# Optimization experiments

Hardware: AMD Instinct MI355X
Metric: run time of the kernel (lower is better)

## Reference

```python
import jax, jax.numpy as jnp
from jax import lax
import numpy as np

FRAME_LEN = 128
HOP = 64  # frame_len // 2 (default hop)
SAMPLE_LEN = 65536
IR_LEN = 1024

# torch.hann_window(N) is periodic: 0.5*(1 - cos(2*pi*n/N))
WIN = 0.5 * (1.0 - jnp.cos(2.0 * jnp.pi * jnp.arange(FRAME_LEN, dtype=jnp.float32) / FRAME_LEN))


def setup_inputs() -> dict:
    key = jax.random.key(0)
    k1, k2 = jax.random.split(key)
    x = jax.random.normal(k1, (1, SAMPLE_LEN), dtype=jnp.float32)
    IR = jax.random.normal(k2, (1, IR_LEN), dtype=jnp.float32)
    return {"x": x, "IR": IR}


def _scale_ir(ir2d):
    # get_MSG + scale_IR(target_gain = MSG + 2)
    spec = jnp.fft.rfft(ir2d[0])
    mag = jnp.abs(spec)
    phase = jnp.angle(spec)
    power = mag ** 2
    MLG = jnp.mean(power)
    zero_phase = (phase > -0.1) & (phase < 0.1)  # DC bin always qualifies
    peak_gain = jnp.max(jnp.where(zero_phase, power, -jnp.inf))
    MSG = -10.0 * jnp.log10(peak_gain / MLG)
    target_gain = MSG + 2.0
    mean_gain = 10.0 * jnp.log10(MLG)
    factor = jnp.power(jnp.float32(0.5), (target_gain - mean_gain) / 6.0)
    return ir2d / factor


def _howling(x1d, ir1d):
    L = x1d.shape[0]
    conv_len = FRAME_LEN + ir1d.shape[0] - 1
    # number of iterations that perform the feedback update (torch loop breaks
    # when frame_start + conv_len >= sample_len, AFTER adding to howling_out)
    n_fb = max(0, (L - conv_len - 1) // HOP)

    def step(x, i):
        fs = i * HOP
        frame = lax.dynamic_slice(x, (fs,), (FRAME_LEN,))
        w = WIN * frame
        conv = jnp.convolve(w, ir1d)  # mode='full', length conv_len
        fs2 = fs + HOP
        seg = lax.dynamic_slice(x, (fs2,), (conv_len,)) + conv
        x = lax.dynamic_update_slice(x, seg, (fs2,))
        x = jnp.clip(x, -1.0, 1.0)
        return x, w

    x_out, frames = lax.scan(step, x1d, jnp.arange(n_fb))
    # last iteration: windowed frame added to howling_out, then break (no feedback, no clamp)
    fs_last = n_fb * HOP
    last_w = WIN * lax.dynamic_slice(x_out, (fs_last,), (FRAME_LEN,))
    frames = jnp.concatenate([frames, last_w[None, :]], axis=0)  # [T, frame_len]
    T = n_fb + 1
    pos = (jnp.arange(T)[:, None] * HOP + jnp.arange(FRAME_LEN)[None, :]).reshape(-1)
    howl = jnp.zeros((L,), x1d.dtype).at[pos].add(frames.reshape(-1))
    return jnp.clip(howl, -1.0, 1.0)


def reference(x, IR):
    ir = _scale_ir(IR)
    out = _howling(x[0], ir[0])
    return out[None, :]
```

## Files before the change

### kernel.cpp

```cpp
#include <hip/hip_runtime.h>
#include <math.h>

#define FRAME 128
#define HOPW 64
#define SLEN 65536
#define IRLEN 1024
#define NFB 1006
#define RMASK 2047
#define PI_D 3.14159265358979323846

__device__ __forceinline__ float clip1(float v) { return fminf(1.0f, fmaxf(-1.0f, v)); }

__device__ __forceinline__ void loop_barrier() {
    __builtin_amdgcn_sched_barrier(0);
    asm volatile("s_waitcnt lgkmcnt(0)" ::: "memory");
    __builtin_amdgcn_s_barrier();
    __builtin_amdgcn_sched_barrier(0);
}

__global__ __launch_bounds__(768) void howl_fused(const float* __restrict__ x,
                                                  const float* __restrict__ ir,
                                                  float* __restrict__ out) {
    __shared__ __align__(16) float ring[2048];
    __shared__ __align__(16) float part[4][1152];
    __shared__ float irl[IRLEN];
    __shared__ float wlds[FRAME];
    __shared__ float red1[1024];
    __shared__ float red2[1024];
    __shared__ float invfs;

    const int tid = threadIdx.x;
    const int lane = tid & 63;
    const int wvid = tid >> 6;
    const int kg = tid / 192;
    const int ob = tid % 192;
    const int q = ob * 6;
    const int lo = q - kg * 32 - 31;

    for (int idx = tid; idx < IRLEN; idx += 768) irl[idx] = ir[idx];
    for (int idx = tid; idx < 1216; idx += 768) ring[idx] = x[idx];
    if (tid >= 513) { red1[tid] = -INFINITY; red2[tid] = 0.f; }
    if (tid < 256) { red1[768 + tid] = -INFINITY; red2[768 + tid] = 0.f; }
    __syncthreads();

    if (tid < 513) {
        double th = -2.0 * PI_D * (double)tid / 1024.0;
        double c4 = cos(4.0 * th), s4 = sin(4.0 * th);
        double wr0 = 1.0,           wi0 = 0.0;
        double wr1 = cos(th),       wi1 = sin(th);
        double wr2 = cos(2.0 * th), wi2 = sin(2.0 * th);
        double wr3 = cos(3.0 * th), wi3 = sin(3.0 * th);
        double ar0 = 0, ai0 = 0, ar1 = 0, ai1 = 0, ar2 = 0, ai2 = 0, ar3 = 0, ai3 = 0;
        for (int m = 0; m < 256; ++m) {
            double x0 = irl[4 * m], x1 = irl[4 * m + 1], x2 = irl[4 * m + 2], x3 = irl[4 * m + 3];
            ar0 += x0 * wr0; ai0 += x0 * wi0;
            ar1 += x1 * wr1; ai1 += x1 * wi1;
            ar2 += x2 * wr2; ai2 += x2 * wi2;
            ar3 += x3 * wr3; ai3 += x3 * wi3;
            double t;
            t = wr0 * c4 - wi0 * s4; wi0 = wr0 * s4 + wi0 * c4; wr0 = t;
            t = wr1 * c4 - wi1 * s4; wi1 = wr1 * s4 + wi1 * c4; wr1 = t;
            t = wr2 * c4 - wi2 * s4; wi2 = wr2 * s4 + wi2 * c4; wr2 = t;
            t = wr3 * c4 - wi3 * s4; wi3 = wr3 * s4 + wi3 * c4; wr3 = t;
        }
        double re = (ar0 + ar1) + (ar2 + ar3);
        double im = (ai0 + ai1) + (ai2 + ai3);
        float mag = (float)sqrt(re * re + im * im);
        float pw = mag * mag;
        double ph = atan2(im, re);
        int ok = (ph > -0.1 && ph < 0.1) ? 1 : 0;
        red1[tid] = ok ? pw : -INFINITY;
        red2[tid] = pw;
    }
    __syncthreads();
    for (int st = 512; st > 0; st >>= 1) {
        if (tid < st) {
            red1[tid] = fmaxf(red1[tid], red1[tid + st]);
            red2[tid] = red2[tid] + red2[tid + st];
        }
        __syncthreads();
    }
    if (tid == 0) {
        float peak = red1[0];
        float MLG = red2[0] / 513.0f;
        float MSG = -10.0f * log10f(peak / MLG);
        float target_gain = MSG + 2.0f;
        float mean_gain = 10.0f * log10f(MLG);
        invfs = powf(0.5f, (target_gain - mean_gain) / 6.0f);
    }
    __syncthreads();
    const float fbc = invfs;

    float wir[37];
#pragma unroll
    for (int j = 0; j < 37; ++j) {
        int idx = lo + j;
        wir[j] = (idx >= 0 && idx < IRLEN) ? irl[idx] / fbc : 0.f;
    }

    const float hvs = (float)(0.5 * (1.0 - cos(PI_D * (double)(tid & 127) / 64.0)));

    float tl = 0.f, xv = 0.f;
    if (tid < FRAME) wlds[tid] = hvs * ring[tid];
    if (wvid == 11) xv = x[1216 + lane];
    if (wvid < 2) __builtin_amdgcn_s_setprio(1);
    __syncthreads();

#pragma unroll 1
    for (int i = 0; i < NFB; ++i) {
        const int base = i * HOPW;

        if (wvid == 0) {
            float w0v = wlds[lane];
            float w1v = wlds[64 + lane];
            out[base + lane] = clip1(w0v + tl);
            tl = w1v;
        } else if (wvid == 11) {
            int pos = base + 1216 + lane;
            if (pos < SLEN) ring[pos & RMASK] = clip1(xv);
            int np = pos + HOPW;
            xv = (np < SLEN) ? x[np] : 0.f;
        }

        float wreg = wlds[kg * 32 + (lane & 31)];
        float a0 = 0, a1 = 0, a2 = 0, a3 = 0, a4 = 0, a5 = 0;
#pragma unroll
        for (int kk = 0; kk < 32; ++kk) {
            float sc = __int_as_float(__builtin_amdgcn_readlane(__float_as_int(wreg), 31 - kk));
            a0 = fmaf(sc, wir[kk + 0], a0);
            a1 = fmaf(sc, wir[kk + 1], a1);
            a2 = fmaf(sc, wir[kk + 2], a2);
            a3 = fmaf(sc, wir[kk + 3], a3);
            a4 = fmaf(sc, wir[kk + 4], a4);
            a5 = fmaf(sc, wir[kk + 5], a5);
        }
        float* pw = &part[kg][q];
        *(float2*)(pw + 0) = make_float2(a0, a1);
        *(float2*)(pw + 2) = make_float2(a2, a3);
        *(float2*)(pw + 4) = make_float2(a4, a5);

        loop_barrier();

        if (tid < 128) {
            int s = tid;
            int slot = (base + 64 + s) & RMASK;
            float rr = ring[slot];
            float sc4 = ((part[0][s] + part[1][s]) + part[2][s]) + part[3][s];
            float v = clip1(rr + sc4);
            ring[slot] = v;
            wlds[s] = hvs * v;
        } else if (tid < 384) {
            int p = 128 + 4 * (tid - 128);
            float4 g0 = *(const float4*)&part[0][p];
            float4 g1 = *(const float4*)&part[1][p];
            float4 g2 = *(const float4*)&part[2][p];
            float4 g3 = *(const float4*)&part[3][p];
            int slot = (base + 64 + p) & RMASK;
            float4 rv = *(float4*)&ring[slot];
            rv.x = clip1(rv.x + (((g0.x + g1.x) + g2.x) + g3.x));
            rv.y = clip1(rv.y + (((g0.y + g1.y) + g2.y) + g3.y));
            rv.z = clip1(rv.z + (((g0.z + g1.z) + g2.z) + g3.z));
            rv.w = clip1(rv.w + (((g0.w + g1.w) + g2.w) + g3.w));
            *(float4*)&ring[slot] = rv;
        }

        loop_barrier();
    }

    if (wvid == 0) {
        out[64384 + lane] = clip1(wlds[lane] + tl);
        out[64448 + lane] = clip1(wlds[64 + lane]);
    }
    for (int idx = 64512 + tid; idx < SLEN; idx += 768) out[idx] = 0.f;
}

extern "C" void kernel_launch(void* const* d_in, const int* in_sizes, int n_in,
                              void* d_out, int out_size, void* d_ws, size_t ws_size,
                              hipStream_t stream) {
    const float* x = (const float*)d_in[0];
    const float* ir = (const float*)d_in[1];
    float* out = (float*)d_out;
    (void)d_ws; (void)ws_size; (void)in_sizes; (void)n_in; (void)out_size;

    hipLaunchKernelGGL(howl_fused, dim3(1), dim3(768), 0, stream, x, ir, out);
}
```

Before: 1.020 ms.

## Double-buffer partial sums to use one barrier per feedback iteration

Restructures the serial feedback loop so each iteration has a single barrier instead of two. The partial-sum buffer is double-buffered. Every thread recomputes the reduced windowed sample it needs straight from the previous partials, which removes the separate reduce-then-broadcast phase. The loop is unrolled by two to ping-pong the buffers. The cost is redundant reduction work in every thread, extra LDS, and subtle ring/vbuf ordering hazards.

```diff
diff --git a/kernel.cpp b/kernel.cpp
--- a/kernel.cpp
+++ b/kernel.cpp
@@ -22,9 +22,10 @@
                                                   const float* __restrict__ ir,
                                                   float* __restrict__ out) {
     __shared__ __align__(16) float ring[2048];
-    __shared__ __align__(16) float part[4][1152];
+    __shared__ __align__(16) float part[2][4][1152];
     __shared__ float irl[IRLEN];
-    __shared__ float wlds[FRAME];
+    __shared__ float vbuf[2][128];
+    __shared__ float wb[2][128];
     __shared__ float red1[1024];
     __shared__ float red2[1024];
     __shared__ float invfs;
@@ -36,6 +37,8 @@
     const int ob = tid % 192;
     const int q = ob * 6;
     const int lo = q - kg * 32 - 31;
+    const int s = kg * 32 + (lane & 31);
+    const bool wlow = (ob < 64) && (lane < 32);
 
     for (int idx = tid; idx < IRLEN; idx += 768) irl[idx] = ir[idx];
     for (int idx = tid; idx < 1216; idx += 768) ring[idx] = x[idx];
@@ -98,31 +101,16 @@
         wir[j] = (idx >= 0 && idx < IRLEN) ? irl[idx] / fbc : 0.f;
     }
 
-    const float hvs = (float)(0.5 * (1.0 - cos(PI_D * (double)(tid & 127) / 64.0)));
-
+    const float hann_s = (float)(0.5 * (1.0 - cos(PI_D * (double)s / 64.0)));
+
+    float wreg = hann_s * ring[s];
+    if (wlow) wb[0][s] = wreg;
+    if (tid < 64) vbuf[1][64 + tid] = ring[64 + tid];
     float tl = 0.f, xv = 0.f;
-    if (tid < FRAME) wlds[tid] = hvs * ring[tid];
     if (wvid == 11) xv = x[1216 + lane];
-    if (wvid < 2) __builtin_amdgcn_s_setprio(1);
-    __syncthreads();
-
-#pragma unroll 1
-    for (int i = 0; i < NFB; ++i) {
-        const int base = i * HOPW;
-
-        if (wvid == 0) {
-            float w0v = wlds[lane];
-            float w1v = wlds[64 + lane];
-            out[base + lane] = clip1(w0v + tl);
-            tl = w1v;
-        } else if (wvid == 11) {
-            int pos = base + 1216 + lane;
-            if (pos < SLEN) ring[pos & RMASK] = clip1(xv);
-            int np = pos + HOPW;
-            xv = (np < SLEN) ? x[np] : 0.f;
-        }
-
-        float wreg = wlds[kg * 32 + (lane & 31)];
+    __syncthreads();
+
+    {
         float a0 = 0, a1 = 0, a2 = 0, a3 = 0, a4 = 0, a5 = 0;
 #pragma unroll
         for (int kk = 0; kk < 32; ++kk) {
@@ -134,27 +122,36 @@
             a4 = fmaf(sc, wir[kk + 4], a4);
             a5 = fmaf(sc, wir[kk + 5], a5);
         }
-        float* pw = &part[kg][q];
+        float* pw = &part[0][kg][q];
         *(float2*)(pw + 0) = make_float2(a0, a1);
         *(float2*)(pw + 2) = make_float2(a2, a3);
         *(float2*)(pw + 4) = make_float2(a4, a5);
-
-        loop_barrier();
-
-        if (tid < 128) {
-            int s = tid;
-            int slot = (base + 64 + s) & RMASK;
-            float rr = ring[slot];
-            float sc4 = ((part[0][s] + part[1][s]) + part[2][s]) + part[3][s];
-            float v = clip1(rr + sc4);
-            ring[slot] = v;
-            wlds[s] = hvs * v;
-        } else if (tid < 384) {
+    }
+    loop_barrier();
+
+    auto body = [&](int i, const float* cur, float* nxt,
+                    const float* vb_r, float* vb_w,
+                    const float* wb_r, float* wb_w) {
+        const int base = i * HOPW;
+
+        if (wvid == 0) {
+            float w0v = wb_r[lane];
+            float w1v = wb_r[64 + lane];
+            out[base + lane] = clip1(w0v + tl);
+            tl = w1v;
+        } else if (wvid == 11) {
+            int pos = base + 1216 + lane;
+            if (pos < SLEN) ring[pos & RMASK] = clip1(xv);
+            int np = pos + HOPW;
+            xv = (np < SLEN) ? x[np] : 0.f;
+        }
+
+        if (tid >= 128 && tid < 384) {
             int p = 128 + 4 * (tid - 128);
-            float4 g0 = *(const float4*)&part[0][p];
-            float4 g1 = *(const float4*)&part[1][p];
-            float4 g2 = *(const float4*)&part[2][p];
-            float4 g3 = *(const float4*)&part[3][p];
+            float4 g0 = *(const float4*)&cur[p];
+            float4 g1 = *(const float4*)&cur[1152 + p];
+            float4 g2 = *(const float4*)&cur[2304 + p];
+            float4 g3 = *(const float4*)&cur[3456 + p];
             int slot = (base + 64 + p) & RMASK;
             float4 rv = *(float4*)&ring[slot];
             rv.x = clip1(rv.x + (((g0.x + g1.x) + g2.x) + g3.x));
@@ -164,12 +161,46 @@
             *(float4*)&ring[slot] = rv;
         }
 
+        {
+            float c0 = cur[s], c1 = cur[1152 + s], c2 = cur[2304 + s], c3 = cur[3456 + s];
+            float rr = (kg < 2) ? vb_r[64 + s] : ring[(base + 64 + s) & RMASK];
+            float v = clip1(rr + (((c0 + c1) + c2) + c3));
+            float wn = hann_s * v;
+            if (kg >= 2 && wlow) vb_w[s] = v;
+            if (wlow) wb_w[s] = wn;
+            wreg = wn;
+        }
+
+        float a0 = 0, a1 = 0, a2 = 0, a3 = 0, a4 = 0, a5 = 0;
+#pragma unroll
+        for (int kk = 0; kk < 32; ++kk) {
+            float sc = __int_as_float(__builtin_amdgcn_readlane(__float_as_int(wreg), 31 - kk));
+            a0 = fmaf(sc, wir[kk + 0], a0);
+            a1 = fmaf(sc, wir[kk + 1], a1);
+            a2 = fmaf(sc, wir[kk + 2], a2);
+            a3 = fmaf(sc, wir[kk + 3], a3);
+            a4 = fmaf(sc, wir[kk + 4], a4);
+            a5 = fmaf(sc, wir[kk + 5], a5);
+        }
+        float* pw = nxt + kg * 1152 + q;
+        *(float2*)(pw + 0) = make_float2(a0, a1);
+        *(float2*)(pw + 2) = make_float2(a2, a3);
+        *(float2*)(pw + 4) = make_float2(a4, a5);
+
         loop_barrier();
+    };
+
+    const float* P0 = &part[0][0][0];
+    float* P1 = &part[1][0][0];
+#pragma unroll 1
+    for (int i = 0; i < NFB; i += 2) {
+        body(i,     P0, (float*)P1, vbuf[1], vbuf[0], wb[0], wb[1]);
+        body(i + 1, P1, (float*)P0, vbuf[0], vbuf[1], wb[1], wb[0]);
     }
 
     if (wvid == 0) {
-        out[64384 + lane] = clip1(wlds[lane] + tl);
-        out[64448 + lane] = clip1(wlds[64 + lane]);
+        out[64384 + lane] = clip1(wb[0][lane] + tl);
+        out[64448 + lane] = clip1(wb[0][64 + lane]);
     }
     for (int idx = 64512 + tid; idx < SLEN; idx += 768) out[idx] = 0.f;
 }
```

New measurement: 1.024 ms. No clear change (+0.4%).
